# Kernel optimization log

Measured on AMD Instinct MI355X. Metric: run time of the kernel, lower is better.

## Reference

```python
import jax, jax.numpy as jnp
import numpy as np

S, I, H = 4096, 1024, 1024  # seq_len, input_size, hidden_size


def setup_inputs() -> dict:
    key = jax.random.key(0)
    ks = jax.random.split(key, 5)
    scale = 1.0 / np.sqrt(H + I)  # nn.Linear default U(-1/sqrt(fan_in), 1/sqrt(fan_in))
    def lin_w(k):
        return jax.random.uniform(k, (4 * H, H + I), jnp.float32, -scale, scale)
    kb1, kb2 = jax.random.split(ks[4])
    return {
        "inputs": jax.random.normal(ks[0], (S, I), jnp.float32),
        # rows stacked as [f; i; g; o] gates, columns as [h | x] (matches cat([h, x]))
        "fwd_W": lin_w(ks[1]),
        "fwd_b": jax.random.uniform(kb1, (4 * H,), jnp.float32, -scale, scale),
        "bwd_W": lin_w(ks[2]),
        "bwd_b": jax.random.uniform(kb2, (4 * H,), jnp.float32, -scale, scale),
    }


def _run_direction(inputs, W, b, reverse):
    # W: (4H, H+I); split into recurrent part (acts on h) and input part (acts on x)
    Wh = W[:, :H]            # (4H, H)
    Wx = W[:, H:]            # (4H, I)
    # Precompute input contribution for all timesteps in one big GEMM: (S, 4H)
    x_proj = inputs @ Wx.T + b

    def step(carry, xp):
        h, c = carry
        z = Wh @ h + xp                          # (4H,)
        f, i, g, o = jnp.split(z, 4)
        c_t = jax.nn.sigmoid(f) * c + jax.nn.sigmoid(i) * jnp.tanh(g)
        h_t = jax.nn.sigmoid(o) * jnp.tanh(c_t)
        return (h_t, c_t), h_t

    h0 = jnp.zeros((H,), inputs.dtype)
    (h_final, _), hs = jax.lax.scan(step, (h0, h0), x_proj, reverse=reverse)
    # scan with reverse=True emits stacked outputs in original (forward) order
    return hs, h_final


def reference(inputs, fwd_W, fwd_b, bwd_W, bwd_b):
    f_hs, f_h = _run_direction(inputs, fwd_W, fwd_b, reverse=False)
    b_hs, b_h = _run_direction(inputs, bwd_W, bwd_b, reverse=True)
    all_hidden = jnp.concatenate([f_hs, b_hs], axis=-1)   # (S, 2H)
    final_h = jnp.concatenate([f_h, b_h], axis=-1)        # (2H,)
    return (all_hidden, final_h)
```

## Files before the change

### kernel.cpp

```cpp
#include <hip/hip_runtime.h>
#include <hip/hip_bf16.h>
#include <cstdint>
#include <cstddef>


typedef __attribute__((ext_vector_type(8))) short short8;
typedef __attribute__((ext_vector_type(4))) short short4v;
typedef __attribute__((ext_vector_type(4))) float float4v;
typedef unsigned long long ull;

__device__ __forceinline__ float bf2f(unsigned short u) {
    return __uint_as_float(((unsigned int)u) << 16);
}
__device__ __forceinline__ unsigned short f2bf(float f) {
    __hip_bfloat16 h = __float2bfloat16(f);
    return *reinterpret_cast<unsigned short*>(&h);
}
__device__ __forceinline__ float sigm(float x) {
    return 1.f / (1.f + __expf(-x));
}
__device__ __forceinline__ float tanh_fast(float x) {
    return 1.f - 2.f / (__expf(2.f * x) + 1.f);
}

__global__ __launch_bounds__(256)
void xproj_gemm(const float* __restrict__ inp,
                const float* __restrict__ fw,
                const float* __restrict__ fb,
                const float* __restrict__ bw,
                const float* __restrict__ bb,
                float* __restrict__ xp)
{
    const int d  = blockIdx.z;
    const float* W = d ? bw : fw;
    const float* B = d ? bb : fb;
    const int t0 = blockIdx.y * 128;
    const int n0 = blockIdx.x * 128;

    __shared__ __align__(16) short Ash[128 * 32];
    __shared__ __align__(16) short Bsh[128 * 32];

    const int tid  = threadIdx.x;
    const int lane = tid & 63;
    const int wave = tid >> 6;
    const int wm = (wave & 1) * 64;
    const int wn = (wave >> 1) * 64;
    const int quad = lane >> 4;
    const int l15  = lane & 15;

    float4v acc[4][4];
    float4v zero4 = {0.f, 0.f, 0.f, 0.f};
#pragma unroll
    for (int mi = 0; mi < 4; mi++)
#pragma unroll
        for (int ni = 0; ni < 4; ni++) acc[mi][ni] = zero4;

    for (int k0 = 0; k0 < 1024; k0 += 32) {
#pragma unroll
        for (int s = 0; s < 4; s++) {
            int c   = tid + s * 256;
            int row = c >> 3;
            int ko  = (c & 7) * 4;
            float4v va = *(const float4v*)&inp[(size_t)(t0 + row) * 1024 + k0 + ko];
            float4v vb = *(const float4v*)&W[(size_t)(n0 + row) * 2048 + 1024 + k0 + ko];
            short4v sa, sb;
#pragma unroll
            for (int e = 0; e < 4; e++) {
                sa[e] = (short)f2bf(va[e]);
                sb[e] = (short)f2bf(vb[e]);
            }
            *(short4v*)&Ash[row * 32 + ko] = sa;
            *(short4v*)&Bsh[row * 32 + ko] = sb;
        }
        __syncthreads();

        short8 af[4], bfr[4];
#pragma unroll
        for (int mi = 0; mi < 4; mi++)
            af[mi] = *(const short8*)&Ash[(wm + mi * 16 + l15) * 32 + quad * 8];
#pragma unroll
        for (int ni = 0; ni < 4; ni++)
            bfr[ni] = *(const short8*)&Bsh[(wn + ni * 16 + l15) * 32 + quad * 8];

#pragma unroll
        for (int mi = 0; mi < 4; mi++)
#pragma unroll
            for (int ni = 0; ni < 4; ni++)
                acc[mi][ni] = __builtin_amdgcn_mfma_f32_16x16x32_bf16(
                    af[mi], bfr[ni], acc[mi][ni], 0, 0, 0);
        __syncthreads();
    }

#pragma unroll
    for (int ni = 0; ni < 4; ni++) {
        int gc = n0 + wn + ni * 16 + l15;
        float bias = B[gc];
#pragma unroll
        for (int mi = 0; mi < 4; mi++) {
#pragma unroll
            for (int r = 0; r < 4; r++) {
                int gr = t0 + wm + mi * 16 + quad * 4 + r;
                xp[((size_t)d * 4096 + gr) * 4096 + gc] = acc[mi][ni][r] + bias;
            }
        }
    }
}

template <int FUSED>
__global__ __launch_bounds__(512, 2)
void lstm_rec(const float* __restrict__ fw,
              const float* __restrict__ bw,
              const float* __restrict__ fb,
              const float* __restrict__ bb,
              const float* __restrict__ inp,
              const float* __restrict__ xp,
              ull* __restrict__ hq,
              float* __restrict__ out)
{
    const int dir  = blockIdx.x & 1;
    const int slot = blockIdx.x >> 1;
    const int u0   = slot * 16;
    const int T    = threadIdx.x;
    const int rl   = T & 63;
    const int gate = rl >> 4;
    const int ul   = rl & 15;
    const int chunk = T >> 6;
    const int j    = gate * 1024 + u0 + ul;
    const float* W = dir ? bw : fw;

    __shared__ __align__(16) float hsh[1024];
    __shared__ __align__(16) float xsh[1024];
    __shared__ float xvs[2][64];
    __shared__ float psum[2][64 * 9];

    float w[128];
    {
        const float* wr = W + (size_t)j * 2048 + chunk * 128;
#pragma unroll
        for (int i = 0; i < 32; i++)
            *(float4v*)&w[4 * i] = *(const float4v*)&wr[4 * i];
    }

    unsigned int w2[64];
    float bj4[4];
    if (FUSED) {
        const float* wr2 = W + (size_t)j * 2048 + 1024 + chunk * 128;
#pragma unroll
        for (int i = 0; i < 32; i++) {
            float4v v = *(const float4v*)&wr2[4 * i];
            w2[2 * i]     = (unsigned int)f2bf(v[0]) | ((unsigned int)f2bf(v[1]) << 16);
            w2[2 * i + 1] = (unsigned int)f2bf(v[2]) | ((unsigned int)f2bf(v[3]) << 16);
        }
        if (T < 16) {
#pragma unroll
            for (int g = 0; g < 4; g++)
                bj4[g] = (dir ? bb : fb)[g * 1024 + u0 + T];
        }
    }

    ull* hqd = hq + dir * 2048;
    float c = 0.f;

    for (int t = 0; t < 4096; t++) {
        const int tr  = dir ? (4095 - t) : t;
        const int par = t & 1;

        float xv = 0.f;
        float2 iv;
        if (FUSED) {
            iv = ((const float2*)&inp[(size_t)tr * 1024])[T];
        } else if (T < 64) {
            xv = xp[((size_t)dir * 4096 + tr) * 4096 + j];
        }

        {
            ull* q0 = &hqd[par * 1024 + 2 * T];
            ull w0 = __hip_atomic_load(q0, __ATOMIC_RELAXED, __HIP_MEMORY_SCOPE_AGENT);
            ull w1 = __hip_atomic_load(q0 + 1, __ATOMIC_RELAXED, __HIP_MEMORY_SCOPE_AGENT);
            while ((unsigned)(w0 >> 32) != (unsigned)t)
                w0 = __hip_atomic_load(q0, __ATOMIC_RELAXED, __HIP_MEMORY_SCOPE_AGENT);
            while ((unsigned)(w1 >> 32) != (unsigned)t)
                w1 = __hip_atomic_load(q0 + 1, __ATOMIC_RELAXED, __HIP_MEMORY_SCOPE_AGENT);
            hsh[2 * T]     = __uint_as_float((unsigned)w0);
            hsh[2 * T + 1] = __uint_as_float((unsigned)w1);
        }
        if (FUSED) {
            xsh[2 * T]     = iv.x;
            xsh[2 * T + 1] = iv.y;
        } else if (T < 64) {
            xvs[par][T] = xv;
        }
        __syncthreads();

        float a0 = 0.f, a1 = 0.f, a2 = 0.f, a3 = 0.f;
        const float4v* h4 = (const float4v*)&hsh[chunk * 128];
#pragma unroll
        for (int i = 0; i < 32; i++) {
            float4v hv = h4[i];
            a0 = __builtin_fmaf(w[4 * i + 0], hv.x, a0);
            a1 = __builtin_fmaf(w[4 * i + 1], hv.y, a1);
            a2 = __builtin_fmaf(w[4 * i + 2], hv.z, a2);
            a3 = __builtin_fmaf(w[4 * i + 3], hv.w, a3);
        }
        if (FUSED) {
            const float* xs = &xsh[chunk * 128];
#pragma unroll
            for (int i = 0; i < 64; i++) {
                unsigned int dv = w2[i];
                a0 = __builtin_fmaf(bf2f((unsigned short)(dv & 0xffffu)),
                                    xs[2 * i], a0);
                a1 = __builtin_fmaf(bf2f((unsigned short)(dv >> 16)),
                                    xs[2 * i + 1], a1);
            }
        }
        psum[par][rl * 9 + chunk] = (a0 + a1) + (a2 + a3);
        __syncthreads();

        if (T < 16) {
            float z[4];
#pragma unroll
            for (int g = 0; g < 4; g++) {
                int row = g * 16 + T;
                float s = FUSED ? bj4[g] : xvs[par][row];
                const float* pp = &psum[par][row * 9];
#pragma unroll
                for (int cc = 0; cc < 8; cc++) s += pp[cc];
                z[g] = s;
            }
            c = sigm(z[0]) * c + sigm(z[1]) * tanh_fast(z[2]);
            float hv = sigm(z[3]) * tanh_fast(c);
            out[(size_t)tr * 2048 + dir * 1024 + u0 + T] = hv;
            if (t == 4095)
                out[(size_t)4096 * 2048 + dir * 1024 + u0 + T] = hv;
            __hip_atomic_store(&hqd[((t + 1) & 1) * 1024 + u0 + T],
                               ((ull)(unsigned)(t + 1) << 32) | __float_as_uint(hv),
                               __ATOMIC_RELAXED, __HIP_MEMORY_SCOPE_AGENT);
        }
    }
}

extern "C" void kernel_launch(void* const* d_in, const int* in_sizes, int n_in,
                              void* d_out, int out_size, void* d_ws, size_t ws_size,
                              hipStream_t stream)
{
    const float* inp = (const float*)d_in[0];
    const float* fw  = (const float*)d_in[1];
    const float* fb  = (const float*)d_in[2];
    const float* bw  = (const float*)d_in[3];
    const float* bb  = (const float*)d_in[4];

    char* ws = (char*)d_ws;
    ull* hq   = (ull*)ws;
    float* xp = (float*)(ws + 32768);

    const size_t XP_BYTES = 2ull * 4096 * 4096 * 4;
    const int have_xp = (ws_size >= 32768 + XP_BYTES);

    hipMemsetAsync(ws, 0, 32768, stream);

    float* outp = (float*)d_out;
    if (have_xp) {
        dim3 gg(32, 32, 2);
        xproj_gemm<<<gg, 256, 0, stream>>>(inp, fw, fb, bw, bb, xp);
        lstm_rec<0><<<dim3(128), 512, 0, stream>>>(fw, bw, fb, bb, inp, xp,
                                                   hq, outp);
    } else {
        lstm_rec<1><<<dim3(128), 512, 0, stream>>>(fw, bw, fb, bb, inp, nullptr,
                                                   hq, outp);
    }
}
```

Baseline: 9.343 ms.

## Split recurrent LSTM across 256 blocks of 256 threads, 8 units each

Doubles the number of persistent recurrent blocks, from 128 to 256, so each handles 8 hidden units instead of 16 and has fewer threads. Each thread now polls and loads 4 hidden values with float4 LDS stores. The gate reduction uses shuffles across 32 threads instead of one thread per unit looping over 4 gates. The aim is to spread the per-step matvec across all 256 CUs for more compute and bandwidth per step. The risk is that more blocks poll the global h buffer, which raises synchronization traffic, and all 256 blocks must be co-resident or the spin-wait deadlocks.

```diff
diff --git a/kernel.cpp b/kernel.cpp
--- a/kernel.cpp
+++ b/kernel.cpp
@@ -107,7 +107,7 @@
 }
 
 template <int FUSED>
-__global__ __launch_bounds__(512, 2)
+__global__ __launch_bounds__(256, 1)
 void lstm_rec(const float* __restrict__ fw,
               const float* __restrict__ bw,
               const float* __restrict__ fb,
@@ -119,19 +119,18 @@
 {
     const int dir  = blockIdx.x & 1;
     const int slot = blockIdx.x >> 1;
-    const int u0   = slot * 16;
+    const int u0   = slot * 8;
     const int T    = threadIdx.x;
-    const int rl   = T & 63;
-    const int gate = rl >> 4;
-    const int ul   = rl & 15;
-    const int chunk = T >> 6;
+    const int rl   = T & 31;
+    const int gate = rl >> 3;
+    const int ul   = rl & 7;
+    const int chunk = T >> 5;
     const int j    = gate * 1024 + u0 + ul;
     const float* W = dir ? bw : fw;
 
     __shared__ __align__(16) float hsh[1024];
     __shared__ __align__(16) float xsh[1024];
-    __shared__ float xvs[2][64];
-    __shared__ float psum[2][64 * 9];
+    __shared__ float psum[2][32 * 9];
 
     float w[128];
     {
@@ -142,7 +141,7 @@
     }
 
     unsigned int w2[64];
-    float bj4[4];
+    float brow = 0.f;
     if (FUSED) {
         const float* wr2 = W + (size_t)j * 2048 + 1024 + chunk * 128;
 #pragma unroll
@@ -151,11 +150,8 @@
             w2[2 * i]     = (unsigned int)f2bf(v[0]) | ((unsigned int)f2bf(v[1]) << 16);
             w2[2 * i + 1] = (unsigned int)f2bf(v[2]) | ((unsigned int)f2bf(v[3]) << 16);
         }
-        if (T < 16) {
-#pragma unroll
-            for (int g = 0; g < 4; g++)
-                bj4[g] = (dir ? bb : fb)[g * 1024 + u0 + T];
-        }
+        if (T < 32)
+            brow = (dir ? bb : fb)[(T >> 3) * 1024 + u0 + (T & 7)];
     }
 
     ull* hqd = hq + dir * 2048;
@@ -166,30 +162,36 @@
         const int par = t & 1;
 
         float xv = 0.f;
-        float2 iv;
+        float4v iv4;
         if (FUSED) {
-            iv = ((const float2*)&inp[(size_t)tr * 1024])[T];
-        } else if (T < 64) {
+            iv4 = ((const float4v*)&inp[(size_t)tr * 1024])[T];
+        } else if (T < 32) {
             xv = xp[((size_t)dir * 4096 + tr) * 4096 + j];
         }
 
         {
-            ull* q0 = &hqd[par * 1024 + 2 * T];
-            ull w0 = __hip_atomic_load(q0, __ATOMIC_RELAXED, __HIP_MEMORY_SCOPE_AGENT);
-            ull w1 = __hip_atomic_load(q0 + 1, __ATOMIC_RELAXED, __HIP_MEMORY_SCOPE_AGENT);
-            while ((unsigned)(w0 >> 32) != (unsigned)t)
-                w0 = __hip_atomic_load(q0, __ATOMIC_RELAXED, __HIP_MEMORY_SCOPE_AGENT);
-            while ((unsigned)(w1 >> 32) != (unsigned)t)
-                w1 = __hip_atomic_load(q0 + 1, __ATOMIC_RELAXED, __HIP_MEMORY_SCOPE_AGENT);
-            hsh[2 * T]     = __uint_as_float((unsigned)w0);
-            hsh[2 * T + 1] = __uint_as_float((unsigned)w1);
-        }
-        if (FUSED) {
-            xsh[2 * T]     = iv.x;
-            xsh[2 * T + 1] = iv.y;
-        } else if (T < 64) {
-            xvs[par][T] = xv;
-        }
+            ull* q0 = &hqd[par * 1024 + 4 * T];
+            ull b0 = __hip_atomic_load(q0,     __ATOMIC_RELAXED, __HIP_MEMORY_SCOPE_AGENT);
+            ull b1 = __hip_atomic_load(q0 + 1, __ATOMIC_RELAXED, __HIP_MEMORY_SCOPE_AGENT);
+            ull b2 = __hip_atomic_load(q0 + 2, __ATOMIC_RELAXED, __HIP_MEMORY_SCOPE_AGENT);
+            ull b3 = __hip_atomic_load(q0 + 3, __ATOMIC_RELAXED, __HIP_MEMORY_SCOPE_AGENT);
+            while ((unsigned)(b0 >> 32) != (unsigned)t)
+                b0 = __hip_atomic_load(q0,     __ATOMIC_RELAXED, __HIP_MEMORY_SCOPE_AGENT);
+            while ((unsigned)(b1 >> 32) != (unsigned)t)
+                b1 = __hip_atomic_load(q0 + 1, __ATOMIC_RELAXED, __HIP_MEMORY_SCOPE_AGENT);
+            while ((unsigned)(b2 >> 32) != (unsigned)t)
+                b2 = __hip_atomic_load(q0 + 2, __ATOMIC_RELAXED, __HIP_MEMORY_SCOPE_AGENT);
+            while ((unsigned)(b3 >> 32) != (unsigned)t)
+                b3 = __hip_atomic_load(q0 + 3, __ATOMIC_RELAXED, __HIP_MEMORY_SCOPE_AGENT);
+            float4v hv4;
+            hv4[0] = __uint_as_float((unsigned)b0);
+            hv4[1] = __uint_as_float((unsigned)b1);
+            hv4[2] = __uint_as_float((unsigned)b2);
+            hv4[3] = __uint_as_float((unsigned)b3);
+            *(float4v*)&hsh[4 * T] = hv4;
+        }
+        if (FUSED)
+            *(float4v*)&xsh[4 * T] = iv4;
         __syncthreads();
 
         float a0 = 0.f, a1 = 0.f, a2 = 0.f, a3 = 0.f;
@@ -216,25 +218,29 @@
         psum[par][rl * 9 + chunk] = (a0 + a1) + (a2 + a3);
         __syncthreads();
 
-        if (T < 16) {
-            float z[4];
-#pragma unroll
-            for (int g = 0; g < 4; g++) {
-                int row = g * 16 + T;
-                float s = FUSED ? bj4[g] : xvs[par][row];
-                const float* pp = &psum[par][row * 9];
+        if (T < 64) {
+            float s = 0.f;
+            if (T < 32) {
+                s = FUSED ? brow : xv;
+                const float* pp = &psum[par][T * 9];
 #pragma unroll
                 for (int cc = 0; cc < 8; cc++) s += pp[cc];
-                z[g] = s;
-            }
-            c = sigm(z[0]) * c + sigm(z[1]) * tanh_fast(z[2]);
-            float hv = sigm(z[3]) * tanh_fast(c);
-            out[(size_t)tr * 2048 + dir * 1024 + u0 + T] = hv;
-            if (t == 4095)
-                out[(size_t)4096 * 2048 + dir * 1024 + u0 + T] = hv;
-            __hip_atomic_store(&hqd[((t + 1) & 1) * 1024 + u0 + T],
-                               ((ull)(unsigned)(t + 1) << 32) | __float_as_uint(hv),
-                               __ATOMIC_RELAXED, __HIP_MEMORY_SCOPE_AGENT);
+            }
+            const int sl = T & 7;
+            float z0 = __shfl(s, sl);
+            float z1 = __shfl(s, sl + 8);
+            float z2 = __shfl(s, sl + 16);
+            float z3 = __shfl(s, sl + 24);
+            if (T < 8) {
+                c = sigm(z0) * c + sigm(z1) * tanh_fast(z2);
+                float hv = sigm(z3) * tanh_fast(c);
+                out[(size_t)tr * 2048 + dir * 1024 + u0 + T] = hv;
+                if (t == 4095)
+                    out[(size_t)4096 * 2048 + dir * 1024 + u0 + T] = hv;
+                __hip_atomic_store(&hqd[((t + 1) & 1) * 1024 + u0 + T],
+                                   ((ull)(unsigned)(t + 1) << 32) | __float_as_uint(hv),
+                                   __ATOMIC_RELAXED, __HIP_MEMORY_SCOPE_AGENT);
+            }
         }
     }
 }
@@ -262,10 +268,10 @@
     if (have_xp) {
         dim3 gg(32, 32, 2);
         xproj_gemm<<<gg, 256, 0, stream>>>(inp, fw, fb, bw, bb, xp);
-        lstm_rec<0><<<dim3(128), 512, 0, stream>>>(fw, bw, fb, bb, inp, xp,
+        lstm_rec<0><<<dim3(256), 256, 0, stream>>>(fw, bw, fb, bb, inp, xp,
                                                    hq, outp);
     } else {
-        lstm_rec<1><<<dim3(128), 512, 0, stream>>>(fw, bw, fb, bb, inp, nullptr,
+        lstm_rec<1><<<dim3(256), 256, 0, stream>>>(fw, bw, fb, bb, inp, nullptr,
                                                    hq, outp);
     }
 }
```

Result: slower. 11.56 ms (+23.7%).

## Drop per-step barrier before matvec and spread gate reduction over 64 lanes

Applied to the files above, without the earlier changes.

Each wavefront now reads only the slice of h and x that its own lanes wrote into shared memory. That lets the block-wide barrier before the matvec become a local LDS wait count. The final gate reduction is spread across 64 threads with cross-lane shuffles instead of 16 threads doing serial sums, and the bias is kept per row. The spin-wait on the hidden-state flags now polls both words in one loop with a short s_sleep. This may add a little wake-up latency on each step of the serial recurrence.

```diff
diff --git a/kernel.cpp b/kernel.cpp
--- a/kernel.cpp
+++ b/kernel.cpp
@@ -130,7 +130,6 @@
 
     __shared__ __align__(16) float hsh[1024];
     __shared__ __align__(16) float xsh[1024];
-    __shared__ float xvs[2][64];
     __shared__ float psum[2][64 * 9];
 
     float w[128];
@@ -142,7 +141,7 @@
     }
 
     unsigned int w2[64];
-    float bj4[4];
+    float brow = 0.f;
     if (FUSED) {
         const float* wr2 = W + (size_t)j * 2048 + 1024 + chunk * 128;
 #pragma unroll
@@ -151,11 +150,8 @@
             w2[2 * i]     = (unsigned int)f2bf(v[0]) | ((unsigned int)f2bf(v[1]) << 16);
             w2[2 * i + 1] = (unsigned int)f2bf(v[2]) | ((unsigned int)f2bf(v[3]) << 16);
         }
-        if (T < 16) {
-#pragma unroll
-            for (int g = 0; g < 4; g++)
-                bj4[g] = (dir ? bb : fb)[g * 1024 + u0 + T];
-        }
+        if (T < 64)
+            brow = (dir ? bb : fb)[(T >> 4) * 1024 + u0 + (T & 15)];
     }
 
     ull* hqd = hq + dir * 2048;
@@ -164,6 +160,7 @@
     for (int t = 0; t < 4096; t++) {
         const int tr  = dir ? (4095 - t) : t;
         const int par = t & 1;
+        const unsigned ut = (unsigned)t;
 
         float xv = 0.f;
         float2 iv;
@@ -175,22 +172,21 @@
 
         {
             ull* q0 = &hqd[par * 1024 + 2 * T];
-            ull w0 = __hip_atomic_load(q0, __ATOMIC_RELAXED, __HIP_MEMORY_SCOPE_AGENT);
+            ull w0 = __hip_atomic_load(q0,     __ATOMIC_RELAXED, __HIP_MEMORY_SCOPE_AGENT);
             ull w1 = __hip_atomic_load(q0 + 1, __ATOMIC_RELAXED, __HIP_MEMORY_SCOPE_AGENT);
-            while ((unsigned)(w0 >> 32) != (unsigned)t)
-                w0 = __hip_atomic_load(q0, __ATOMIC_RELAXED, __HIP_MEMORY_SCOPE_AGENT);
-            while ((unsigned)(w1 >> 32) != (unsigned)t)
+            while ((unsigned)(w0 >> 32) != ut || (unsigned)(w1 >> 32) != ut) {
+                __builtin_amdgcn_s_sleep(1);
+                w0 = __hip_atomic_load(q0,     __ATOMIC_RELAXED, __HIP_MEMORY_SCOPE_AGENT);
                 w1 = __hip_atomic_load(q0 + 1, __ATOMIC_RELAXED, __HIP_MEMORY_SCOPE_AGENT);
+            }
             hsh[2 * T]     = __uint_as_float((unsigned)w0);
             hsh[2 * T + 1] = __uint_as_float((unsigned)w1);
         }
         if (FUSED) {
             xsh[2 * T]     = iv.x;
             xsh[2 * T + 1] = iv.y;
-        } else if (T < 64) {
-            xvs[par][T] = xv;
-        }
-        __syncthreads();
+        }
+        asm volatile("s_waitcnt lgkmcnt(0)" ::: "memory");
 
         float a0 = 0.f, a1 = 0.f, a2 = 0.f, a3 = 0.f;
         const float4v* h4 = (const float4v*)&hsh[chunk * 128];
@@ -216,25 +212,26 @@
         psum[par][rl * 9 + chunk] = (a0 + a1) + (a2 + a3);
         __syncthreads();
 
-        if (T < 16) {
-            float z[4];
-#pragma unroll
-            for (int g = 0; g < 4; g++) {
-                int row = g * 16 + T;
-                float s = FUSED ? bj4[g] : xvs[par][row];
-                const float* pp = &psum[par][row * 9];
-#pragma unroll
-                for (int cc = 0; cc < 8; cc++) s += pp[cc];
-                z[g] = s;
-            }
-            c = sigm(z[0]) * c + sigm(z[1]) * tanh_fast(z[2]);
-            float hv = sigm(z[3]) * tanh_fast(c);
-            out[(size_t)tr * 2048 + dir * 1024 + u0 + T] = hv;
-            if (t == 4095)
-                out[(size_t)4096 * 2048 + dir * 1024 + u0 + T] = hv;
-            __hip_atomic_store(&hqd[((t + 1) & 1) * 1024 + u0 + T],
-                               ((ull)(unsigned)(t + 1) << 32) | __float_as_uint(hv),
-                               __ATOMIC_RELAXED, __HIP_MEMORY_SCOPE_AGENT);
+        if (T < 64) {
+            float s = FUSED ? brow : xv;
+            const float* pp = &psum[par][T * 9];
+#pragma unroll
+            for (int cc = 0; cc < 8; cc++) s += pp[cc];
+            const int u = T & 15;
+            float z0 = __shfl(s, u);
+            float z1 = __shfl(s, u + 16);
+            float z2 = __shfl(s, u + 32);
+            float z3 = __shfl(s, u + 48);
+            if (T < 16) {
+                c = sigm(z0) * c + sigm(z1) * tanh_fast(z2);
+                float hv = sigm(z3) * tanh_fast(c);
+                out[(size_t)tr * 2048 + dir * 1024 + u0 + T] = hv;
+                if (t == 4095)
+                    out[(size_t)4096 * 2048 + dir * 1024 + u0 + T] = hv;
+                __hip_atomic_store(&hqd[((t + 1) & 1) * 1024 + u0 + T],
+                                   ((ull)(unsigned)(t + 1) << 32) | __float_as_uint(hv),
+                                   __ATOMIC_RELAXED, __HIP_MEMORY_SCOPE_AGENT);
+            }
         }
     }
 }
```

Result: faster. 8.690 ms (-7.0%).
